# Performance work log

Measured on AMD Instinct MI355X. Metric: run time of the kernel, lower is better.

## Reference

```python
import jax, jax.numpy as jnp
import numpy as np

# graph sizes
G, P, EP = 128, 256, 1024          # graphs, nodes/graph, edges/graph
N, E = G * P, G * EP
C, KENS, S = 4, 2, 1               # centroids, ensembles, samples
R = S * KENS                       # repeats
F, DE, D, OUT = 64, 16, 128, 10


def setup_inputs() -> dict:
    key = jax.random.key(0)
    ks = jax.random.split(key, 24)
    off = (jnp.arange(G, dtype=jnp.int32) * P)[:, None]
    src = (jax.random.randint(ks[0], (G, EP), 0, P, dtype=jnp.int32) + off).reshape(-1)
    dst = (jax.random.randint(ks[1], (G, EP), 0, P, dtype=jnp.int32) + off).reshape(-1)
    edge_index = jnp.stack([src, dst])            # [2, E], edges stay within graphs
    batch = jnp.repeat(jnp.arange(G, dtype=jnp.int32), P)  # [N]
    rn = lambda k, shp, s: jax.random.normal(k, shp, jnp.float32) * s
    return {
        "x_feat": rn(ks[2], (N, F), 1.0),
        "edge_attr": rn(ks[3], (E, DE), 1.0),
        "W_atom": rn(ks[4], (F, D), 0.1), "b_atom": jnp.zeros((D,), jnp.float32),
        "W_score": rn(ks[5], (D, C * KENS), 0.1),
        "W_edge": rn(ks[6], (DE, D), 0.1),
        "W_b2c": rn(ks[7], (D, D), 0.1),
        "W_bb": rn(ks[8], (D, D), 0.1), "W_bc": rn(ks[9], (D, D), 0.1),
        "W_cb": rn(ks[10], (D, D), 0.1), "W_cc": rn(ks[11], (D, D), 0.1),
        "W_sb": rn(ks[12], (D, D), 0.1), "W_sc": rn(ks[13], (D, D), 0.1),
        "W_inter": rn(ks[14], (D, D), 0.1), "b_inter": jnp.zeros((D,), jnp.float32),
        "W_out": rn(ks[15], (D, OUT), 0.1), "b_out": jnp.zeros((OUT,), jnp.float32),
        "edge_index": edge_index, "batch": batch,
    }


def reference(x_feat, edge_attr, W_atom, b_atom, W_score, W_edge, W_b2c,
              W_bb, W_bc, W_cb, W_cc, W_sb, W_sc, W_inter, b_inter,
              W_out, b_out, edge_index, batch):
    src, dst = edge_index[0], edge_index[1]
    # atom encoder + scorer + softmax sampler (marginals)
    x = x_feat @ W_atom + b_atom                                  # [N,D]
    scores = (x @ W_score).reshape(N, C, KENS)
    marg = jax.nn.softmax(scores, axis=1)                         # over centroids
    nm = jnp.broadcast_to(marg[None], (S, N, C, KENS))            # [S,N,C,KENS]
    nm = jnp.transpose(nm, (0, 3, 2, 1)).reshape(R, C, N)         # [R,C,N]
    em = nm[:, :, src] * nm[:, :, dst]                            # edge_mask [R,C,E]
    # base2centroid: masked MP on base graph + weighted segment-mean pooling
    edge_emb = edge_attr @ W_edge                                 # [E,D]
    h = jax.nn.relu(x @ W_b2c)                                    # [N,D]
    m = h[src] + edge_emb                                         # [E,D]
    agg = jnp.zeros((R, C, N, D), m.dtype).at[:, :, dst].add(em[..., None] * m)
    hm = h[None, None] + agg                                      # [R,C,N,D]
    denom = jnp.zeros((R, C, G), nm.dtype).at[:, :, batch].add(nm)
    num = jnp.zeros((R, C, G, D), hm.dtype).at[:, :, batch].add(nm[..., None] * hm)
    cent_x = jnp.transpose(num / (denom[..., None] + 1e-6), (0, 2, 1, 3))  # [R,G,C,D]
    # intra centroid-pair edge weights: triu pairs + diag, scatter over graphs
    iu, ju = np.triu_indices(C, 1)
    pi = np.concatenate([iu, np.arange(C)])
    pj = np.concatenate([ju, np.arange(C)])
    e2g = batch[src]
    w = jnp.zeros((R, pi.size, G), nm.dtype).at[:, :, e2g].add(
        nm[:, pi][:, :, src] * nm[:, pj][:, :, dst])              # [R,10,G]
    w = w.at[:, -C:, :].multiply(0.5)                             # halve diagonal counts
    wt = jnp.transpose(w, (0, 2, 1))                              # [R,G,10]
    Wcc = jnp.zeros((R, G, C, C), nm.dtype)
    Wcc = Wcc.at[:, :, pi, pj].add(wt).at[:, :, pj, pi].add(wt)   # to_undirected
    dg = jnp.arange(C)
    Wcc = Wcc.at[:, :, dg, dg].multiply(0.5)                      # self loops counted once
    Wcc = Wcc / (jax.lax.stop_gradient(jnp.max(Wcc)) + 1e-9)      # detached-max norm
    # hetero GNN layer: base->base, base->centroid, centroid->centroid, centroid->base
    agg_bb = jnp.zeros((N, D), x.dtype).at[dst].add(x[src] + edge_emb)           # [N,D]
    agg_bc = jnp.transpose(
        jnp.zeros((R, C, G, D), x.dtype).at[:, :, batch].add(nm[..., None] * x[None, None]),
        (0, 2, 1, 3))                                             # [R,G,C,D]
    agg_cc = jnp.einsum('rgij,rgjd->rgid', Wcc, cent_x)
    h_cent = jax.nn.relu(agg_bc @ W_bc + agg_cc @ W_cc + cent_x @ W_sc)          # [R,G,C,D]
    agg_cb = jnp.einsum('rcn,rncd->rnd', nm, h_cent[:, batch])                   # [R,N,D]
    h_base = jax.nn.relu(agg_bb[None] @ W_bb + agg_cb @ W_cb + x[None] @ W_sb)   # [R,N,D]
    # inter-ensemble mean pool, inter head, intra mean graph pool, intra head
    node_emb = jnp.mean(h_base, axis=0) @ W_inter + b_inter                      # [N,D]
    graph_emb = jnp.zeros((G, D), node_emb.dtype).at[batch].add(node_emb) / P    # [G,D]
    return graph_emb @ W_out + b_out                                             # [G,OUT]
```

## Files before the change

### kernel.cpp

```cpp
#include <hip/hip_runtime.h>
#include <hip/hip_bf16.h>

#define Nn 32768
#define Ee 131072
#define Gg 128
#define Dd 128

using bf16 = __hip_bfloat16;
typedef __attribute__((ext_vector_type(8))) short bf16x8;
typedef __attribute__((ext_vector_type(4))) float f32x4;

__device__ __forceinline__ float b2f(bf16 v){ return __bfloat162float(v); }
__device__ __forceinline__ bf16  f2b(float v){ return __float2bfloat16(v); }
__device__ __forceinline__ unsigned short bf16bits(float v){
  union { bf16 b; unsigned short u; } cv; cv.b = f2b(v); return cv.u;
}
__device__ __forceinline__ float bfu(unsigned short u){
  return __uint_as_float((unsigned int)u << 16);
}
__device__ __forceinline__ float upk_x(unsigned int v){ return __uint_as_float(v << 16); }
__device__ __forceinline__ float upk_h(unsigned int v){ return __uint_as_float(v & 0xffff0000u); }

__global__ __launch_bounds__(128)
void k_wrep(const float* __restrict__ Wbb, const float* __restrict__ Wsb,
            const float* __restrict__ Wcb, const float* __restrict__ Wa,
            const float* __restrict__ Wb2c,
            unsigned short* __restrict__ Wbbp, unsigned short* __restrict__ Wsbp,
            unsigned short* __restrict__ Wcbp, unsigned short* __restrict__ Wap,
            unsigned short* __restrict__ Wb2cp) {
  int mat = blockIdx.x >> 7, n = blockIdx.x & 127, k = threadIdx.x;
  if      (mat == 0) Wbbp [n*128 + k] = bf16bits(Wbb [k*128 + n]);
  else if (mat == 1) Wsbp [n*128 + k] = bf16bits(Wsb [k*128 + n]);
  else if (mat == 2) Wcbp [n*128 + k] = bf16bits(Wcb [k*128 + n]);
  else if (mat == 3) { if (k < 64) Wap[n*64 + k] = bf16bits(Wa[k*128 + n]); }
  else               Wb2cp[n*128 + k] = bf16bits(Wb2c[k*128 + n]);
}

__global__ __launch_bounds__(256)
void k_atom(const float* __restrict__ xf, const unsigned short* __restrict__ Wap,
            const float* __restrict__ ba, const float* __restrict__ Wsc,
            const unsigned short* __restrict__ Wb2cp,
            unsigned int* __restrict__ xh, float* __restrict__ nmt) {
  __shared__ unsigned short sxf[64*72];
  __shared__ unsigned short sxb[64*136];
  __shared__ float ss[64*8];
  __shared__ float sWsc[1024];
  int tid = threadIdx.x, n0 = blockIdx.x*64;
  int lane = tid & 63, wv = tid >> 6;
  int m = lane & 15, quad = lane >> 4;
  int rbase = wv*16;
  #pragma unroll
  for (int k = 0; k < 4; ++k) {
    int pos = (tid + k*256)*4;
    int node = pos >> 6, f = pos & 63;
    float4 v = *reinterpret_cast<const float4*>(xf + (size_t)n0*64 + pos);
    ushort4 o;
    o.x = bf16bits(v.x); o.y = bf16bits(v.y); o.z = bf16bits(v.z); o.w = bf16bits(v.w);
    *reinterpret_cast<ushort4*>(&sxf[node*72 + f]) = o;
  }
  for (int j = tid; j < 1024; j += 256) sWsc[j] = Wsc[j];
  __syncthreads();
  f32x4 cx[8];
  #pragma unroll
  for (int nt = 0; nt < 8; ++nt) {
    float bv = ba[nt*16 + m];
    cx[nt] = (f32x4){bv, bv, bv, bv};
  }
  const unsigned short* a1 = &sxf[(rbase + m)*72];
  #pragma unroll
  for (int nt = 0; nt < 8; ++nt) {
    #pragma unroll
    for (int kk = 0; kk < 2; ++kk) {
      int ko = kk*32 + quad*8;
      bf16x8 av = *reinterpret_cast<const bf16x8*>((const short*)a1 + ko);
      bf16x8 bv8 = *reinterpret_cast<const bf16x8*>((const short*)Wap + (nt*16 + m)*64 + ko);
      cx[nt] = __builtin_amdgcn_mfma_f32_16x16x32_bf16(av, bv8, cx[nt], 0, 0, 0);
    }
  }
  #pragma unroll
  for (int nt = 0; nt < 8; ++nt)
    #pragma unroll
    for (int i = 0; i < 4; ++i)
      sxb[(rbase + quad*4 + i)*136 + nt*16 + m] = bf16bits(cx[nt][i]);
  __syncthreads();
  for (int p = tid; p < 512; p += 256) {
    int node = p >> 3, col = p & 7;
    float s = 0.f;
    for (int dd = 0; dd < 128; ++dd)
      s += bfu(sxb[node*136 + dd]) * sWsc[dd*8 + col];
    ss[node*8 + col] = s;
  }
  __syncthreads();
  if (tid < 128) {
    int node = tid >> 1, k = tid & 1;
    float v0 = ss[node*8 + 0 + k], v1 = ss[node*8 + 2 + k];
    float v2 = ss[node*8 + 4 + k], v3 = ss[node*8 + 6 + k];
    float mx = fmaxf(fmaxf(v0, v1), fmaxf(v2, v3));
    float e0 = expf(v0-mx), e1 = expf(v1-mx), e2 = expf(v2-mx), e3 = expf(v3-mx);
    float inv = 1.f / (e0+e1+e2+e3);
    *reinterpret_cast<float4*>(nmt + (size_t)(n0 + node)*8 + k*4) =
        make_float4(e0*inv, e1*inv, e2*inv, e3*inv);
  }
  f32x4 chf[8];
  #pragma unroll
  for (int nt = 0; nt < 8; ++nt) chf[nt] = (f32x4){0.f,0.f,0.f,0.f};
  const unsigned short* a2 = &sxb[(rbase + m)*136];
  #pragma unroll
  for (int nt = 0; nt < 8; ++nt) {
    #pragma unroll
    for (int kk = 0; kk < 4; ++kk) {
      int ko = kk*32 + quad*8;
      bf16x8 av = *reinterpret_cast<const bf16x8*>((const short*)a2 + ko);
      bf16x8 bv8 = *reinterpret_cast<const bf16x8*>((const short*)Wb2cp + (nt*16 + m)*128 + ko);
      chf[nt] = __builtin_amdgcn_mfma_f32_16x16x32_bf16(av, bv8, chf[nt], 0, 0, 0);
    }
  }
  #pragma unroll
  for (int nt = 0; nt < 8; ++nt) {
    #pragma unroll
    for (int i = 0; i < 4; ++i) {
      int row = rbase + quad*4 + i, col = nt*16 + m;
      float hv = fmaxf(chf[nt][i], 0.f);
      unsigned short xb = sxb[row*136 + col];
      xh[(size_t)(n0 + row)*128 + col] =
          ((unsigned int)bf16bits(hv) << 16) | (unsigned int)xb;
    }
  }
}

__global__ __launch_bounds__(256)
void k_gedge(const int* __restrict__ ei, const float* __restrict__ nmt,
             const float* __restrict__ ea,
             int* __restrict__ osrc, int* __restrict__ rowstart,
             float* __restrict__ sea, float* __restrict__ den,
             float* __restrict__ bnmp, float* __restrict__ geap,
             float* __restrict__ wsump) {
  __shared__ __align__(16) char smem[42576];
  int t = threadIdx.x;
  if (blockIdx.x < Gg) {
    int g = blockIdx.x;
    int* cnt    = (int*)smem;
    int* off    = cnt + 256;
    int* sdl    = off + 256;
    int* ssl    = sdl + 1024;
    int* sorder = ssl + 1024;
    float* den8 = (float*)(sorder + 1024);
    cnt[t] = 0;
    if (t < 8) den8[t] = 0.f;
    __syncthreads();
    #pragma unroll
    for (int j = 0; j < 4; ++j) {
      int e = t + j*256;
      int sl = ei[g*1024 + e] - g*256;
      int dl = ei[Ee + g*1024 + e] - g*256;
      ssl[e] = sl; sdl[e] = dl;
      atomicAdd(&cnt[dl], 1);
    }
    {
      const float4* p = reinterpret_cast<const float4*>(nmt + (size_t)(g*256 + t)*8);
      float4 a = p[0], b = p[1];
      float v[8] = {a.x,a.y,a.z,a.w,b.x,b.y,b.z,b.w};
      #pragma unroll
      for (int i = 0; i < 8; ++i) {
        float s = v[i];
        for (int o = 32; o > 0; o >>= 1) s += __shfl_xor(s, o);
        if ((t & 63) == 0) atomicAdd(&den8[i], s);
      }
    }
    __syncthreads();
    off[t] = cnt[t];
    __syncthreads();
    for (int s = 1; s < 256; s <<= 1) {
      int v = (t >= s) ? off[t - s] : 0;
      __syncthreads();
      off[t] += v;
      __syncthreads();
    }
    int startv = off[t] - cnt[t];
    int mycnt = cnt[t];
    rowstart[g*256 + t] = startv;
    off[t] = startv;
    __syncthreads();
    #pragma unroll
    for (int j = 0; j < 4; ++j) {
      int e = t + j*256;
      int pos = atomicAdd(&off[sdl[e]], 1);
      osrc[g*1024 + pos] = g*256 + ssl[e];
      sorder[pos] = e;
    }
    __syncthreads();
    float s0x=0,s0y=0,s0z=0,s0w=0, s1x=0,s1y=0,s1z=0,s1w=0;
    float s2x=0,s2y=0,s2z=0,s2w=0, s3x=0,s3y=0,s3z=0,s3w=0;
    for (int jj = startv; jj < startv + mycnt; ++jj) {
      int e = sorder[jj];
      const float4* er = reinterpret_cast<const float4*>(ea + ((size_t)g*1024 + e)*16);
      float4 a0 = er[0], a1 = er[1], a2 = er[2], a3 = er[3];
      s0x+=a0.x; s0y+=a0.y; s0z+=a0.z; s0w+=a0.w;
      s1x+=a1.x; s1y+=a1.y; s1z+=a1.z; s1w+=a1.w;
      s2x+=a2.x; s2y+=a2.y; s2z+=a2.z; s2w+=a2.w;
      s3x+=a3.x; s3y+=a3.y; s3z+=a3.z; s3w+=a3.w;
    }
    float4* so = reinterpret_cast<float4*>(sea + (size_t)(g*256 + t)*16);
    so[0] = make_float4(s0x,s0y,s0z,s0w);
    so[1] = make_float4(s1x,s1y,s1z,s1w);
    so[2] = make_float4(s2x,s2y,s2z,s2w);
    so[3] = make_float4(s3x,s3y,s3z,s3w);
    if (t < 8) den[t*Gg + g] = den8[t];
  } else {
    int bq = blockIdx.x - Gg;
    float* eaT   = (float*)smem;
    float* salT  = eaT + 16*260;
    float* sbeta = salT + 8*260;
    float* red   = sbeta + 8*260;
    float* sga   = red + 20;
    float* snmt  = sga + 256;
    int g = bq >> 2;
    int ebase = g*1024 + (bq & 3)*256;
    for (int j = t; j < 2080; j += 256) sbeta[j] = 0.f;
    if (t < 20) red[t] = 0.f;
    for (int j = t; j < 2048; j += 256) snmt[j] = nmt[(size_t)g*2048 + j];
    __syncthreads();
    int sl = ei[ebase + t] - g*256;
    int dl = ei[Ee + ebase + t] - g*256;
    const float4* ps4 = reinterpret_cast<const float4*>(snmt + sl*8);
    const float4* pt4 = reinterpret_cast<const float4*>(snmt + dl*8);
    float4 sv0 = ps4[0], sv1 = ps4[1], tv0 = pt4[0], tv1 = pt4[1];
    float ps[8] = {sv0.x,sv0.y,sv0.z,sv0.w,sv1.x,sv1.y,sv1.z,sv1.w};
    float pt[8] = {tv0.x,tv0.y,tv0.z,tv0.w,tv1.x,tv1.y,tv1.z,tv1.w};
    float w20[20];
    #pragma unroll
    for (int r = 0; r < 2; ++r) {
      int b = r*4;
      w20[r*10+0] = ps[b+0]*pt[b+1]; w20[r*10+1] = ps[b+0]*pt[b+2];
      w20[r*10+2] = ps[b+0]*pt[b+3]; w20[r*10+3] = ps[b+1]*pt[b+2];
      w20[r*10+4] = ps[b+1]*pt[b+3]; w20[r*10+5] = ps[b+2]*pt[b+3];
      w20[r*10+6] = ps[b+0]*pt[b+0]; w20[r*10+7] = ps[b+1]*pt[b+1];
      w20[r*10+8] = ps[b+2]*pt[b+2]; w20[r*10+9] = ps[b+3]*pt[b+3];
    }
    #pragma unroll
    for (int rc = 0; rc < 8; ++rc) {
      float al = ps[rc]*pt[rc]*pt[rc];
      salT[rc*260 + t] = al;
      atomicAdd(&sbeta[rc*260 + sl], al);
    }
    {
      const float4* ea4 = reinterpret_cast<const float4*>(ea + (size_t)ebase*16);
      #pragma unroll
      for (int k = 0; k < 4; ++k) {
        float4 v = ea4[t*4 + k];
        eaT[(k*4+0)*260 + t] = v.x;
        eaT[(k*4+1)*260 + t] = v.y;
        eaT[(k*4+2)*260 + t] = v.z;
        eaT[(k*4+3)*260 + t] = v.w;
      }
    }
    #pragma unroll
    for (int i = 0; i < 20; ++i) {
      for (int o = 32; o > 0; o >>= 1) w20[i] += __shfl_down(w20[i], o);
    }
    if ((t & 63) == 0) {
      #pragma unroll
      for (int i = 0; i < 20; ++i) atomicAdd(&red[i], w20[i]);
    }
    __syncthreads();
    {
      int rc = t >> 5, j = (t >> 1) & 15, hf = t & 1;
      float a = 0.f;
      int eb = hf*128;
      for (int ee = eb; ee < eb + 128; ++ee)
        a += salT[rc*260 + ee] * eaT[j*260 + ee];
      sga[t] = a;
    }
    __syncthreads();
    if ((t & 1) == 0) {
      int rc = t >> 5, j = (t >> 1) & 15;
      geap[(size_t)bq*128 + rc*16 + j] = sga[t] + sga[t+1];
    }
    if (t < 20) wsump[bq*20 + t] = red[t];
    {
      float4* bo = reinterpret_cast<float4*>(bnmp + (size_t)bq*2048 + t*8);
      bo[0] = make_float4(sbeta[0*260+t], sbeta[1*260+t], sbeta[2*260+t], sbeta[3*260+t]);
      bo[1] = make_float4(sbeta[4*260+t], sbeta[5*260+t], sbeta[6*260+t], sbeta[7*260+t]);
    }
  }
}

__global__ __launch_bounds__(128)
void k_wfin(const float* __restrict__ wsump, float* __restrict__ wcc,
            float* __restrict__ maxv) {
  __shared__ float smax[128];
  int t = threadIdx.x;
  float w[20];
  #pragma unroll
  for (int i = 0; i < 20; ++i)
    w[i] = wsump[(t*4+0)*20 + i] + wsump[(t*4+1)*20 + i]
         + wsump[(t*4+2)*20 + i] + wsump[(t*4+3)*20 + i];
  float mx = 0.f;
  #pragma unroll
  for (int r = 0; r < 2; ++r) {
    #pragma unroll
    for (int ij = 0; ij < 16; ++ij) {
      int i = ij >> 2, j = ij & 3;
      float v;
      if (i == j) v = 0.5f * w[r*10 + 6 + i];
      else { int a = i < j ? i : j, b = i < j ? j : i;
             int p = (a == 0) ? (b - 1) : (a == 1) ? (b + 1) : 5;
             v = w[r*10 + p]; }
      wcc[(r*Gg + t)*16 + ij] = v;
      mx = fmaxf(mx, v);
    }
  }
  smax[t] = mx;
  __syncthreads();
  for (int s = 64; s > 0; s >>= 1) {
    if (t < s) smax[t] = fmaxf(smax[t], smax[t + s]);
    __syncthreads();
  }
  if (t == 0) maxv[0] = smax[0];
}

__global__ __launch_bounds__(256)
void k_poolagg(const unsigned int* __restrict__ xh, const float* __restrict__ nmt,
               const float* __restrict__ bnmp, const float* __restrict__ sea,
               const float* __restrict__ We, const int* __restrict__ osrc,
               const int* __restrict__ rowstart,
               unsigned short* __restrict__ aggbb16,
               float* __restrict__ pnum, float* __restrict__ pabc) {
  __shared__ unsigned short sxg[256*128];
  int t = threadIdx.x, d = t & 127, q = t >> 7;
  int g = blockIdx.x >> 2, quar = blockIdx.x & 3;
  for (int j = t; j < 32768; j += 256)
    sxg[j] = (unsigned short)(xh[(size_t)(g << 8)*128 + j] & 0xffffu);
  __syncthreads();
  float w[16];
  #pragma unroll
  for (int j = 0; j < 16; ++j) w[j] = We[j*128 + d];
  float aH[8] = {0,0,0,0,0,0,0,0};
  float aX[8] = {0,0,0,0,0,0,0,0};
  int nbase = g*256 + quar*64;
  for (int nn = q; nn < 64; nn += 2) {
    int n = nbase + nn, ln = n & 255;
    unsigned int vn = xh[(size_t)n*128 + d];
    float xn = upk_x(vn), hn = upk_h(vn);
    const float4* pp = reinterpret_cast<const float4*>(nmt + (size_t)n*8);
    float4 p0 = pp[0], p1 = pp[1];
    float pc[8] = {p0.x,p0.y,p0.z,p0.w,p1.x,p1.y,p1.z,p1.w};
    float bt[8] = {0,0,0,0,0,0,0,0};
    #pragma unroll
    for (int qq = 0; qq < 4; ++qq) {
      const float4* bp = reinterpret_cast<const float4*>(bnmp + (size_t)(g*4+qq)*2048 + ln*8);
      float4 b0 = bp[0], b1 = bp[1];
      bt[0]+=b0.x; bt[1]+=b0.y; bt[2]+=b0.z; bt[3]+=b0.w;
      bt[4]+=b1.x; bt[5]+=b1.y; bt[6]+=b1.z; bt[7]+=b1.w;
    }
    #pragma unroll
    for (int rc = 0; rc < 8; ++rc) {
      aH[rc] += (pc[rc] + bt[rc])*hn;
      aX[rc] += pc[rc]*xn;
    }
    const float4* sp = reinterpret_cast<const float4*>(sea + (size_t)n*16);
    float4 s0 = sp[0], s1 = sp[1], s2 = sp[2], s3 = sp[3];
    float agg = s0.x*w[0] + s0.y*w[1] + s0.z*w[2] + s0.w*w[3]
              + s1.x*w[4] + s1.y*w[5] + s1.z*w[6] + s1.w*w[7]
              + s2.x*w[8] + s2.y*w[9] + s2.z*w[10]+ s2.w*w[11]
              + s3.x*w[12]+ s3.y*w[13]+ s3.z*w[14]+ s3.w*w[15];
    int start = rowstart[n];
    int end = (ln == 255) ? 1024 : rowstart[n+1];
    for (int jj = start; jj < end; ++jj) {
      int sg = osrc[g*1024 + jj];
      agg += bfu(sxg[(sg & 255)*128 + d]);
    }
    aggbb16[(size_t)n*128 + d] = bf16bits(agg);
  }
  int slot = quar*2 + q;
  #pragma unroll
  for (int rc = 0; rc < 8; ++rc) {
    pnum[(((size_t)rc*Gg + g)*8 + slot)*128 + d] = aH[rc];
    pabc[(((size_t)rc*Gg + g)*8 + slot)*128 + d] = aX[rc];
  }
}

__global__ __launch_bounds__(128)
void k_hcent(const float* __restrict__ pnum, const float* __restrict__ den,
             const float* __restrict__ pabc, const float* __restrict__ geap,
             const float* __restrict__ We, const float* __restrict__ wcc,
             const float* __restrict__ maxv,
             const float* __restrict__ Wbc, const float* __restrict__ Wcc_,
             const float* __restrict__ Wsc2, float* __restrict__ hcent) {
  __shared__ float scent[512], sbc[512], sccs[512], swcc[16], sgea[64];
  int tid = threadIdx.x, r = blockIdx.x >> 7, g = blockIdx.x & 127;
  float inv = 1.f / (maxv[0] + 1e-9f);
  if (tid < 16) swcc[tid] = wcc[(r*Gg + g)*16 + tid] * inv;
  if (tid < 64) {
    int c = tid >> 4, j = tid & 15;
    int idx = (r*4 + c)*16 + j;
    sgea[tid] = geap[(size_t)(g*4+0)*128 + idx] + geap[(size_t)(g*4+1)*128 + idx]
              + geap[(size_t)(g*4+2)*128 + idx] + geap[(size_t)(g*4+3)*128 + idx];
  }
  __syncthreads();
  for (int c = 0; c < 4; ++c) {
    int rc = r*4 + c;
    float nv = 0.f, av = 0.f;
    #pragma unroll
    for (int s = 0; s < 8; ++s) {
      nv += pnum[(((size_t)rc*Gg + g)*8 + s)*128 + tid];
      av += pabc[(((size_t)rc*Gg + g)*8 + s)*128 + tid];
    }
    #pragma unroll
    for (int j = 0; j < 16; ++j) nv += sgea[c*16 + j] * We[j*128 + tid];
    float dn = den[rc*Gg + g] + 1e-6f;
    scent[c*128 + tid] = nv / dn;
    sbc[c*128 + tid]   = av;
  }
  __syncthreads();
  for (int i = 0; i < 4; ++i) {
    sccs[i*128 + tid] = swcc[i*4+0]*scent[tid]       + swcc[i*4+1]*scent[128 + tid]
                      + swcc[i*4+2]*scent[256 + tid] + swcc[i*4+3]*scent[384 + tid];
  }
  __syncthreads();
  float acc[4] = {0.f, 0.f, 0.f, 0.f};
  for (int k = 0; k < 128; ++k) {
    float wb = Wbc[k*128 + tid], wc = Wcc_[k*128 + tid], ws2 = Wsc2[k*128 + tid];
    #pragma unroll
    for (int c = 0; c < 4; ++c)
      acc[c] += sbc[c*128 + k]*wb + sccs[c*128 + k]*wc + scent[c*128 + k]*ws2;
  }
  #pragma unroll
  for (int c = 0; c < 4; ++c)
    hcent[((r*Gg + g)*4 + c)*128 + tid] = fmaxf(acc[c], 0.f);
}

__global__ __launch_bounds__(256)
void k_hbase(const unsigned short* __restrict__ aggbb16,
             const unsigned int* __restrict__ xh,
             const float* __restrict__ nmt, const float* __restrict__ hcent,
             const unsigned short* __restrict__ Wbbp,
             const unsigned short* __restrict__ Wsbp,
             const unsigned short* __restrict__ Wcbp,
             float* __restrict__ pgsum) {
  __shared__ unsigned short A1[64*136];
  __shared__ unsigned short A2[64*136];
  __shared__ float shc[512];
  __shared__ float snm[256];
  __shared__ float pred[128];
  int tid = threadIdx.x, n0 = blockIdx.x*64, g = n0 >> 8;
  int lane = tid & 63, wv = tid >> 6;
  int m = lane & 15, quad = lane >> 4;
  int rbase = wv*16;
  for (int j = tid; j < 1024; j += 256) {
    int row = j >> 4, col = (j & 15) * 8;
    uint4 v = *reinterpret_cast<const uint4*>(aggbb16 + (size_t)(n0+row)*128 + col);
    *reinterpret_cast<uint4*>(&A1[row*136 + col]) = v;
  }
  for (int j = tid; j < 2048; j += 256) {
    int row = j >> 5, col = (j & 31) * 4;
    uint4 v = *reinterpret_cast<const uint4*>(xh + (size_t)(n0+row)*128 + col);
    uint2 o;
    o.x = (v.x & 0xffffu) | (v.y << 16);
    o.y = (v.z & 0xffffu) | (v.w << 16);
    *reinterpret_cast<uint2*>(&A2[row*136 + col]) = o;
  }
  __syncthreads();
  f32x4 bb[8];
  #pragma unroll
  for (int nt = 0; nt < 8; ++nt) bb[nt] = (f32x4){0.f,0.f,0.f,0.f};
  const short* a1r = (const short*)&A1[(rbase + m)*136];
  const short* a2r = (const short*)&A2[(rbase + m)*136];
  #pragma unroll
  for (int nt = 0; nt < 8; ++nt) {
    #pragma unroll
    for (int kk = 0; kk < 4; ++kk) {
      int ko = kk*32 + quad*8;
      bf16x8 av1 = *reinterpret_cast<const bf16x8*>(a1r + ko);
      bf16x8 wv1 = *reinterpret_cast<const bf16x8*>((const short*)Wbbp + (nt*16 + m)*128 + ko);
      bb[nt] = __builtin_amdgcn_mfma_f32_16x16x32_bf16(av1, wv1, bb[nt], 0, 0, 0);
      bf16x8 av2 = *reinterpret_cast<const bf16x8*>(a2r + ko);
      bf16x8 wv2 = *reinterpret_cast<const bf16x8*>((const short*)Wsbp + (nt*16 + m)*128 + ko);
      bb[nt] = __builtin_amdgcn_mfma_f32_16x16x32_bf16(av2, wv2, bb[nt], 0, 0, 0);
    }
  }
  __syncthreads();
  unsigned short* SB = A2;
  f32x4 msum[8];
  #pragma unroll
  for (int nt = 0; nt < 8; ++nt) msum[nt] = (f32x4){0.f,0.f,0.f,0.f};
  for (int r = 0; r < 2; ++r) {
    for (int j = tid; j < 512; j += 256) shc[j] = hcent[((size_t)(r*Gg + g)*4)*128 + j];
    if (tid < 256) snm[tid] = nmt[(size_t)(n0 + (tid >> 2))*8 + r*4 + (tid & 3)];
    __syncthreads();
    for (int j = tid; j < 8192; j += 256) {
      int node = j >> 7, k = j & 127;
      float v = snm[node*4+0]*shc[k]       + snm[node*4+1]*shc[128 + k]
              + snm[node*4+2]*shc[256 + k] + snm[node*4+3]*shc[384 + k];
      SB[node*136 + k] = bf16bits(v);
    }
    __syncthreads();
    f32x4 aw[8];
    #pragma unroll
    for (int nt = 0; nt < 8; ++nt) aw[nt] = (f32x4){0.f,0.f,0.f,0.f};
    const short* sbr = (const short*)&SB[(rbase + m)*136];
    #pragma unroll
    for (int nt = 0; nt < 8; ++nt) {
      #pragma unroll
      for (int kk = 0; kk < 4; ++kk) {
        int ko = kk*32 + quad*8;
        bf16x8 av = *reinterpret_cast<const bf16x8*>(sbr + ko);
        bf16x8 wvv = *reinterpret_cast<const bf16x8*>((const short*)Wcbp + (nt*16 + m)*128 + ko);
        aw[nt] = __builtin_amdgcn_mfma_f32_16x16x32_bf16(av, wvv, aw[nt], 0, 0, 0);
      }
    }
    #pragma unroll
    for (int nt = 0; nt < 8; ++nt) {
      #pragma unroll
      for (int i = 0; i < 4; ++i)
        msum[nt][i] += 0.5f * fmaxf(bb[nt][i] + aw[nt][i], 0.f);
    }
    __syncthreads();
  }
  if (tid < 128) pred[tid] = 0.f;
  __syncthreads();
  #pragma unroll
  for (int nt = 0; nt < 8; ++nt) {
    float s = msum[nt][0] + msum[nt][1] + msum[nt][2] + msum[nt][3];
    atomicAdd(&pred[nt*16 + m], s);
  }
  __syncthreads();
  if (tid < 128) pgsum[(size_t)blockIdx.x*128 + tid] = pred[tid];
}

__global__ __launch_bounds__(128)
void k_out(const float* __restrict__ pgsum, const float* __restrict__ Wint,
           const float* __restrict__ bint, const float* __restrict__ Wout,
           const float* __restrict__ bout, float* __restrict__ out) {
  __shared__ float ss[128], sge[128];
  int tid = threadIdx.x, g = blockIdx.x;
  float s = pgsum[(size_t)(g*4+0)*128 + tid] + pgsum[(size_t)(g*4+1)*128 + tid]
          + pgsum[(size_t)(g*4+2)*128 + tid] + pgsum[(size_t)(g*4+3)*128 + tid];
  ss[tid] = s * (1.f/256.f);
  __syncthreads();
  float ge = bint[tid];
  for (int k = 0; k < 128; ++k) ge += ss[k] * Wint[k*128 + tid];
  sge[tid] = ge;
  __syncthreads();
  if (tid < 10) {
    float o = bout[tid];
    for (int d = 0; d < 128; ++d) o += sge[d] * Wout[d*10 + tid];
    out[g*10 + tid] = o;
  }
}

extern "C" void kernel_launch(void* const* d_in, const int* in_sizes, int n_in,
                              void* d_out, int out_size, void* d_ws, size_t ws_size,
                              hipStream_t stream) {
  const float* xf   = (const float*)d_in[0];
  const float* ea   = (const float*)d_in[1];
  const float* Wa   = (const float*)d_in[2];
  const float* ba   = (const float*)d_in[3];
  const float* Wsc  = (const float*)d_in[4];
  const float* We   = (const float*)d_in[5];
  const float* Wb2c = (const float*)d_in[6];
  const float* Wbb  = (const float*)d_in[7];
  const float* Wbc  = (const float*)d_in[8];
  const float* Wcb  = (const float*)d_in[9];
  const float* WccW = (const float*)d_in[10];
  const float* Wsb  = (const float*)d_in[11];
  const float* Wsc2 = (const float*)d_in[12];
  const float* Wint = (const float*)d_in[13];
  const float* bint = (const float*)d_in[14];
  const float* Wout = (const float*)d_in[15];
  const float* bout = (const float*)d_in[16];
  const int*   ei   = (const int*)d_in[17];

  float* ws    = (float*)d_ws;
  unsigned int* xh = (unsigned int*)ws;
  float* nmt   = ws + 4194304;
  float* hcent = ws + 4456448;
  float* wcc   = ws + 4587520;
  unsigned short* aggbb16 = (unsigned short*)(ws + 4591616);
  int*   osrc  = (int*)(ws + 6688768);
  int*   rowst = (int*)(ws + 6950912);
  float* sea   = ws + 6983680;
  float* bnmp  = ws + 7507968;
  float* geap  = ws + 8556544;
  float* wsump = ws + 8622080;
  float* pnum  = ws + 8632320;
  float* pabc  = ws + 10729472;
  float* den   = ws + 12826624;
  float* pgsum = ws + 12827648;
  float* maxv  = ws + 12893184;
  unsigned short* Wbbp  = (unsigned short*)(ws + 12893248);
  unsigned short* Wsbp  = (unsigned short*)(ws + 12901440);
  unsigned short* Wcbp  = (unsigned short*)(ws + 12909632);
  unsigned short* Wap   = (unsigned short*)(ws + 12917824);
  unsigned short* Wb2cp = (unsigned short*)(ws + 12921920);

  k_wrep   <<<5*128,   128, 0, stream>>>(Wbb, Wsb, Wcb, Wa, Wb2c,
                                         Wbbp, Wsbp, Wcbp, Wap, Wb2cp);
  k_atom   <<<Nn/64,   256, 0, stream>>>(xf, Wap, ba, Wsc, Wb2cp, xh, nmt);
  k_gedge  <<<Gg+Gg*4, 256, 0, stream>>>(ei, nmt, ea, osrc, rowst, sea, den,
                                         bnmp, geap, wsump);
  k_wfin   <<<1,       128, 0, stream>>>(wsump, wcc, maxv);
  k_poolagg<<<Gg*4,    256, 0, stream>>>(xh, nmt, bnmp, sea, We, osrc, rowst,
                                         aggbb16, pnum, pabc);
  k_hcent  <<<2*Gg,    128, 0, stream>>>(pnum, den, pabc, geap, We, wcc, maxv,
                                         Wbc, WccW, Wsc2, hcent);
  k_hbase  <<<Nn/64,   256, 0, stream>>>(aggbb16, xh, nmt, hcent, Wbbp, Wsbp, Wcbp, pgsum);
  k_out    <<<Gg,      128, 0, stream>>>(pgsum, Wint, bint, Wout, bout, (float*)d_out);
}
```

Measured before the change: 276.3 us.

## Replace per-block full-graph LDS staging with edge-parallel LDS atomic aggregation

k_poolagg no longer copies the whole graph's 256x128 x features into LDS (64KB) for each of its four quarter-blocks. It now scatters only the edges whose destination falls in its quarter, using LDS float atomics into a 64x128 accumulator, and reads x rows straight from global memory. osrc now packs the local destination alongside the source so each edge knows its target row. The four-way bnmp partial sum moves into extra blocks of k_wfin, which writes a per-node bnm buffer that k_poolagg reads once. This cuts LDS footprint, which may allow more blocks per CU, and removes redundant loads, at the cost of LDS atomic contention and uncoalesced global gathers.

```diff
diff --git a/kernel.cpp b/kernel.cpp
--- a/kernel.cpp
+++ b/kernel.cpp
@@ -185,7 +185,7 @@
     for (int j = 0; j < 4; ++j) {
       int e = t + j*256;
       int pos = atomicAdd(&off[sdl[e]], 1);
-      osrc[g*1024 + pos] = g*256 + ssl[e];
+      osrc[g*1024 + pos] = (sdl[e] << 16) | ssl[e];
       sorder[pos] = e;
     }
     __syncthreads();
@@ -285,32 +285,44 @@
   }
 }
 
-__global__ __launch_bounds__(128)
-void k_wfin(const float* __restrict__ wsump, float* __restrict__ wcc,
-            float* __restrict__ maxv) {
+__global__ __launch_bounds__(256)
+void k_wfin(const float* __restrict__ wsump, const float* __restrict__ bnmp,
+            float* __restrict__ wcc, float* __restrict__ maxv,
+            float* __restrict__ bnm) {
+  int t = threadIdx.x;
+  if (blockIdx.x < Gg) {
+    int g = blockIdx.x;
+    for (int j = t; j < 2048; j += 256) {
+      float s = bnmp[(size_t)(g*4+0)*2048 + j] + bnmp[(size_t)(g*4+1)*2048 + j]
+              + bnmp[(size_t)(g*4+2)*2048 + j] + bnmp[(size_t)(g*4+3)*2048 + j];
+      bnm[(size_t)g*2048 + j] = s;
+    }
+    return;
+  }
   __shared__ float smax[128];
-  int t = threadIdx.x;
-  float w[20];
-  #pragma unroll
-  for (int i = 0; i < 20; ++i)
-    w[i] = wsump[(t*4+0)*20 + i] + wsump[(t*4+1)*20 + i]
-         + wsump[(t*4+2)*20 + i] + wsump[(t*4+3)*20 + i];
   float mx = 0.f;
-  #pragma unroll
-  for (int r = 0; r < 2; ++r) {
-    #pragma unroll
-    for (int ij = 0; ij < 16; ++ij) {
-      int i = ij >> 2, j = ij & 3;
-      float v;
-      if (i == j) v = 0.5f * w[r*10 + 6 + i];
-      else { int a = i < j ? i : j, b = i < j ? j : i;
-             int p = (a == 0) ? (b - 1) : (a == 1) ? (b + 1) : 5;
-             v = w[r*10 + p]; }
-      wcc[(r*Gg + t)*16 + ij] = v;
-      mx = fmaxf(mx, v);
-    }
-  }
-  smax[t] = mx;
+  if (t < 128) {
+    float w[20];
+    #pragma unroll
+    for (int i = 0; i < 20; ++i)
+      w[i] = wsump[(t*4+0)*20 + i] + wsump[(t*4+1)*20 + i]
+           + wsump[(t*4+2)*20 + i] + wsump[(t*4+3)*20 + i];
+    #pragma unroll
+    for (int r = 0; r < 2; ++r) {
+      #pragma unroll
+      for (int ij = 0; ij < 16; ++ij) {
+        int i = ij >> 2, j = ij & 3;
+        float v;
+        if (i == j) v = 0.5f * w[r*10 + 6 + i];
+        else { int a = i < j ? i : j, b = i < j ? j : i;
+               int p = (a == 0) ? (b - 1) : (a == 1) ? (b + 1) : 5;
+               v = w[r*10 + p]; }
+        wcc[(r*Gg + t)*16 + ij] = v;
+        mx = fmaxf(mx, v);
+      }
+    }
+    smax[t] = mx;
+  }
   __syncthreads();
   for (int s = 64; s > 0; s >>= 1) {
     if (t < s) smax[t] = fmaxf(smax[t], smax[t + s]);
@@ -321,38 +333,44 @@
 
 __global__ __launch_bounds__(256)
 void k_poolagg(const unsigned int* __restrict__ xh, const float* __restrict__ nmt,
-               const float* __restrict__ bnmp, const float* __restrict__ sea,
+               const float* __restrict__ bnm, const float* __restrict__ sea,
                const float* __restrict__ We, const int* __restrict__ osrc,
                const int* __restrict__ rowstart,
                unsigned short* __restrict__ aggbb16,
                float* __restrict__ pnum, float* __restrict__ pabc) {
-  __shared__ unsigned short sxg[256*128];
+  __shared__ float sagg[64*128];
+  __shared__ int   sopk[512];
   int t = threadIdx.x, d = t & 127, q = t >> 7;
   int g = blockIdx.x >> 2, quar = blockIdx.x & 3;
-  for (int j = t; j < 32768; j += 256)
-    sxg[j] = (unsigned short)(xh[(size_t)(g << 8)*128 + j] & 0xffffu);
+  int nbase = g*256 + quar*64;
+  int rs0 = rowstart[nbase];
+  int rs1 = (quar == 3) ? 1024 : rowstart[nbase + 64];
+  int ecnt = rs1 - rs0;
+  for (int j = t; j < 8192; j += 256) sagg[j] = 0.f;
+  for (int j = t; j < ecnt; j += 256) sopk[j] = osrc[g*1024 + rs0 + j];
+  __syncthreads();
+  for (int jj = q; jj < ecnt; jj += 2) {
+    int pk = sopk[jj];
+    int sl = pk & 255, dl = (pk >> 16) & 255;
+    float xv = upk_x(xh[(size_t)(g*256 + sl)*128 + d]);
+    atomicAdd(&sagg[(dl - quar*64)*128 + d], xv);
+  }
   __syncthreads();
   float w[16];
   #pragma unroll
   for (int j = 0; j < 16; ++j) w[j] = We[j*128 + d];
   float aH[8] = {0,0,0,0,0,0,0,0};
   float aX[8] = {0,0,0,0,0,0,0,0};
-  int nbase = g*256 + quar*64;
   for (int nn = q; nn < 64; nn += 2) {
-    int n = nbase + nn, ln = n & 255;
+    int n = nbase + nn;
     unsigned int vn = xh[(size_t)n*128 + d];
     float xn = upk_x(vn), hn = upk_h(vn);
     const float4* pp = reinterpret_cast<const float4*>(nmt + (size_t)n*8);
     float4 p0 = pp[0], p1 = pp[1];
     float pc[8] = {p0.x,p0.y,p0.z,p0.w,p1.x,p1.y,p1.z,p1.w};
-    float bt[8] = {0,0,0,0,0,0,0,0};
-    #pragma unroll
-    for (int qq = 0; qq < 4; ++qq) {
-      const float4* bp = reinterpret_cast<const float4*>(bnmp + (size_t)(g*4+qq)*2048 + ln*8);
-      float4 b0 = bp[0], b1 = bp[1];
-      bt[0]+=b0.x; bt[1]+=b0.y; bt[2]+=b0.z; bt[3]+=b0.w;
-      bt[4]+=b1.x; bt[5]+=b1.y; bt[6]+=b1.z; bt[7]+=b1.w;
-    }
+    const float4* bp = reinterpret_cast<const float4*>(bnm + (size_t)n*8);
+    float4 b0 = bp[0], b1 = bp[1];
+    float bt[8] = {b0.x,b0.y,b0.z,b0.w,b1.x,b1.y,b1.z,b1.w};
     #pragma unroll
     for (int rc = 0; rc < 8; ++rc) {
       aH[rc] += (pc[rc] + bt[rc])*hn;
@@ -364,12 +382,7 @@
               + s1.x*w[4] + s1.y*w[5] + s1.z*w[6] + s1.w*w[7]
               + s2.x*w[8] + s2.y*w[9] + s2.z*w[10]+ s2.w*w[11]
               + s3.x*w[12]+ s3.y*w[13]+ s3.z*w[14]+ s3.w*w[15];
-    int start = rowstart[n];
-    int end = (ln == 255) ? 1024 : rowstart[n+1];
-    for (int jj = start; jj < end; ++jj) {
-      int sg = osrc[g*1024 + jj];
-      agg += bfu(sxg[(sg & 255)*128 + d]);
-    }
+    agg += sagg[nn*128 + d];
     aggbb16[(size_t)n*128 + d] = bf16bits(agg);
   }
   int slot = quar*2 + q;
@@ -593,14 +606,15 @@
   unsigned short* Wcbp  = (unsigned short*)(ws + 12909632);
   unsigned short* Wap   = (unsigned short*)(ws + 12917824);
   unsigned short* Wb2cp = (unsigned short*)(ws + 12921920);
+  float* bnm   = ws + 12930112;
 
   k_wrep   <<<5*128,   128, 0, stream>>>(Wbb, Wsb, Wcb, Wa, Wb2c,
                                          Wbbp, Wsbp, Wcbp, Wap, Wb2cp);
   k_atom   <<<Nn/64,   256, 0, stream>>>(xf, Wap, ba, Wsc, Wb2cp, xh, nmt);
   k_gedge  <<<Gg+Gg*4, 256, 0, stream>>>(ei, nmt, ea, osrc, rowst, sea, den,
                                          bnmp, geap, wsump);
-  k_wfin   <<<1,       128, 0, stream>>>(wsump, wcc, maxv);
-  k_poolagg<<<Gg*4,    256, 0, stream>>>(xh, nmt, bnmp, sea, We, osrc, rowst,
+  k_wfin   <<<Gg+1,    256, 0, stream>>>(wsump, bnmp, wcc, maxv, bnm);
+  k_poolagg<<<Gg*4,    256, 0, stream>>>(xh, nmt, bnm, sea, We, osrc, rowst,
                                          aggbb16, pnum, pabc);
   k_hcent  <<<2*Gg,    128, 0, stream>>>(pnum, den, pabc, geap, We, wcc, maxv,
                                          Wbc, WccW, Wsc2, hcent);
```

Result: slower. 325.0 us (+17.6%).
